# Optimization experiments

Hardware: AMD Instinct MI355X
Metric: run time of the kernel (lower is better)

## Reference

```python
import jax, jax.numpy as jnp
import numpy as np

N_EMBD = 768
N_HEAD = 12
EPS = 1e-5

def setup_inputs() -> dict:
    key = jax.random.key(0)
    ks = jax.random.split(key, 13)
    C = N_EMBD
    s = lambda n: 1.0 / np.sqrt(n)
    return {
        "x":      jax.random.normal(ks[0], (2, 2048, C), dtype=jnp.float32),
        "ln1_w":  jnp.ones((C,), jnp.float32),
        "ln1_b":  jnp.zeros((C,), jnp.float32),
        "w_qkv":  jax.random.normal(ks[1], (C, 3 * C), dtype=jnp.float32) * s(C),
        "b_qkv":  jnp.zeros((3 * C,), jnp.float32),
        "w_proj": jax.random.normal(ks[2], (C, C), dtype=jnp.float32) * s(C),
        "b_proj": jnp.zeros((C,), jnp.float32),
        "ln2_w":  jnp.ones((C,), jnp.float32),
        "ln2_b":  jnp.zeros((C,), jnp.float32),
        "w_fc1":  jax.random.normal(ks[3], (C, 4 * C), dtype=jnp.float32) * s(C),
        "b_fc1":  jnp.zeros((4 * C,), jnp.float32),
        "w_fc2":  jax.random.normal(ks[4], (4 * C, C), dtype=jnp.float32) * s(4 * C),
        "b_fc2":  jnp.zeros((C,), jnp.float32),
    }

def _layernorm(x, w, b):
    mu = jnp.mean(x, axis=-1, keepdims=True)
    var = jnp.mean(jnp.square(x - mu), axis=-1, keepdims=True)
    return (x - mu) * jax.lax.rsqrt(var + EPS) * w + b

def reference(x, ln1_w, ln1_b, w_qkv, b_qkv, w_proj, b_proj,
              ln2_w, ln2_b, w_fc1, b_fc1, w_fc2, b_fc2):
    B, T, C = x.shape
    H = N_HEAD
    hd = C // H
    # --- attention branch ---
    h = _layernorm(x, ln1_w, ln1_b)
    qkv = h @ w_qkv + b_qkv                                  # [B,T,3C]
    q, k, v = jnp.split(qkv, 3, axis=-1)
    q = q.reshape(B, T, H, hd).transpose(0, 2, 1, 3)          # [B,H,T,hd]
    k = k.reshape(B, T, H, hd).transpose(0, 2, 1, 3)
    v = v.reshape(B, T, H, hd).transpose(0, 2, 1, 3)
    att = jnp.einsum('bhqd,bhkd->bhqk', q, k) * (1.0 / np.sqrt(hd))
    causal = jnp.tril(jnp.ones((T, T), dtype=bool))
    att = jnp.where(causal, att, -jnp.inf)
    att = jax.nn.softmax(att, axis=-1)
    y = jnp.einsum('bhqk,bhkd->bhqd', att, v)                 # [B,H,T,hd]
    y = y.transpose(0, 2, 1, 3).reshape(B, T, C)
    x = x + (y @ w_proj + b_proj)
    # --- MLP branch (dropout = identity in eval) ---
    h = _layernorm(x, ln2_w, ln2_b)
    h = jax.nn.gelu(h @ w_fc1 + b_fc1, approximate=False)
    x = x + (h @ w_fc2 + b_fc2)
    return x
```

## Files before the change

kernel.cpp:

```cpp
#include <hip/hip_runtime.h>
#include <math.h>

typedef __attribute__((ext_vector_type(8))) short short8;
typedef __attribute__((ext_vector_type(4))) float floatx4;

__device__ __forceinline__ unsigned short f2bf(float f) {
    union { float f; unsigned u; } v; v.f = f;
    unsigned r = v.u + 0x7fffu + ((v.u >> 16) & 1u);
    return (unsigned short)(r >> 16);
}

__device__ __forceinline__ float bf2f(unsigned short h) {
    union { unsigned u; float f; } v; v.u = ((unsigned)h) << 16; return v.f;
}

__device__ __forceinline__ float fexp2(float x) {
#if __has_builtin(__builtin_amdgcn_exp2f)
    return __builtin_amdgcn_exp2f(x);
#else
    return __expf(x * 0.69314718056f);
#endif
}

__device__ __forceinline__ void gload16(const unsigned short* g, unsigned short* l) {
    __builtin_amdgcn_global_load_lds(
        (const __attribute__((address_space(1))) unsigned int*)g,
        (__attribute__((address_space(3))) unsigned int*)l, 16, 0, 0);
}

__global__ __launch_bounds__(256) void ln_kernel(const float* __restrict__ x,
                                                 const float* __restrict__ w,
                                                 const float* __restrict__ b,
                                                 unsigned short* __restrict__ o) {
    int row = blockIdx.x, tid = threadIdx.x;
    const float* xr = x + (size_t)row * 768;
    float v0 = xr[tid], v1 = xr[tid + 256], v2 = xr[tid + 512];
    float s = v0 + v1 + v2, ss = v0 * v0 + v1 * v1 + v2 * v2;
#pragma unroll
    for (int o_ = 32; o_; o_ >>= 1) { s += __shfl_xor(s, o_); ss += __shfl_xor(ss, o_); }
    __shared__ float red[8];
    if ((tid & 63) == 0) { red[tid >> 6] = s; red[(tid >> 6) + 4] = ss; }
    __syncthreads();
    s = red[0] + red[1] + red[2] + red[3];
    ss = red[4] + red[5] + red[6] + red[7];
    float mu = s * (1.f / 768.f);
    float var = ss * (1.f / 768.f) - mu * mu;
    float inv = rsqrtf(var + 1e-5f);
    unsigned short* orow = o + (size_t)row * 768;
    orow[tid]       = f2bf((v0 - mu) * inv * w[tid]       + b[tid]);
    orow[tid + 256] = f2bf((v1 - mu) * inv * w[tid + 256] + b[tid + 256]);
    orow[tid + 512] = f2bf((v2 - mu) * inv * w[tid + 512] + b[tid + 512]);
}

__global__ __launch_bounds__(256) void wt_all_kernel(
    const float* __restrict__ w0, unsigned short* __restrict__ t0,
    const float* __restrict__ w1, unsigned short* __restrict__ t1,
    const float* __restrict__ w2, unsigned short* __restrict__ t2,
    const float* __restrict__ w3, unsigned short* __restrict__ t3) {
    int bid = (int)blockIdx.x;
    const float* w; unsigned short* wt; int K, N, bx, by;
    if (bid < 1728)      { w = w0; wt = t0; K = 768;  N = 2304; int l = bid;        bx = l % 72; by = l / 72; }
    else if (bid < 2304) { w = w1; wt = t1; K = 768;  N = 768;  int l = bid - 1728; bx = l % 24; by = l / 24; }
    else if (bid < 4608) { w = w2; wt = t2; K = 768;  N = 3072; int l = bid - 2304; bx = l % 96; by = l / 96; }
    else                 { w = w3; wt = t3; K = 3072; N = 768;  int l = bid - 4608; bx = l % 24; by = l / 24; }
    __shared__ float t[32][33];
    int n0 = bx * 32, k0 = by * 32;
    int tx = threadIdx.x & 31, ty = threadIdx.x >> 5;
#pragma unroll
    for (int i = 0; i < 32; i += 8)
        t[ty + i][tx] = w[(size_t)(k0 + ty + i) * N + n0 + tx];
    __syncthreads();
#pragma unroll
    for (int i = 0; i < 32; i += 8)
        wt[(size_t)(n0 + ty + i) * K + k0 + tx] = f2bf(t[tx][ty + i]);
}

template <int EPI>
__global__ __launch_bounds__(256) void gemm_kernel(
    const unsigned short* __restrict__ A, const unsigned short* __restrict__ Bt,
    const float* __restrict__ bias, const float* __restrict__ resid,
    float* __restrict__ fout, unsigned short* __restrict__ o0,
    unsigned short* __restrict__ o1, unsigned short* __restrict__ o2,
    int K, int Kcnt) {
    __shared__ unsigned short Al[2][128 * 32];
    __shared__ unsigned short Bl[2][128 * 32];
    int tid = threadIdx.x, lane = tid & 63, w = tid >> 6;
    int wm = w >> 1, wn = w & 1;
    int nwg = (int)(gridDim.x * gridDim.y);
    int wgid = (int)(blockIdx.y * gridDim.x + blockIdx.x);
    int logical = (wgid & 7) * (nwg >> 3) + (wgid >> 3);
    int by = logical & 31, bx = logical >> 5;
    int m0 = by * 128;
    int n0, kof = 0, chunk = 0;
    if (EPI == 4) {
        n0 = (bx % 6) * 128;
        chunk = bx / 6;
        kof = chunk * 768;
    } else {
        n0 = bx * 128;
    }
    int lr = lane & 15, lk = (lane >> 4) << 3;

    int srow = w * 32 + (lane >> 2);
    int sko = (lane & 3) << 3;
    const unsigned short* Ab = A + (size_t)(m0 + srow) * K + kof + sko;
    const unsigned short* Bb = Bt + (size_t)(n0 + srow) * K + kof + sko;

    floatx4 acc[4][4];
#pragma unroll
    for (int i = 0; i < 4; i++)
#pragma unroll
        for (int j = 0; j < 4; j++) acc[i][j] = (floatx4){0.f, 0.f, 0.f, 0.f};

    int nk = Kcnt >> 5;
    auto stage = [&](int buf, int t) {
        int k0 = t << 5;
        unsigned short* Alp = &Al[buf][(w * 32) * 32];
        unsigned short* Blp = &Bl[buf][(w * 32) * 32];
        gload16(Ab + k0, Alp);
        gload16(Ab + 16 * K + k0, Alp + 16 * 32);
        gload16(Bb + k0, Blp);
        gload16(Bb + 16 * K + k0, Blp + 16 * 32);
    };

    stage(0, 0);
    for (int t = 0; t < nk; t++) {
        int cur = t & 1;
        __syncthreads();
        if (t + 1 < nk) stage(cur ^ 1, t + 1);
        short8 af[4], bfr[4];
#pragma unroll
        for (int mt = 0; mt < 4; mt++) af[mt] = *(short8*)&Al[cur][(wm * 64 + mt * 16 + lr) * 32 + lk];
#pragma unroll
        for (int nt = 0; nt < 4; nt++) bfr[nt] = *(short8*)&Bl[cur][(wn * 64 + nt * 16 + lr) * 32 + lk];
#pragma unroll
        for (int mt = 0; mt < 4; mt++)
#pragma unroll
            for (int nt = 0; nt < 4; nt++)
                acc[mt][nt] = __builtin_amdgcn_mfma_f32_16x16x32_bf16(af[mt], bfr[nt], acc[mt][nt], 0, 0, 0);
    }

    int mb = m0 + wm * 64, nb = n0 + wn * 64;
    int sec = 0;
    if (EPI == 0) sec = n0 / 768;
#pragma unroll
    for (int mt = 0; mt < 4; mt++)
#pragma unroll
        for (int nt = 0; nt < 4; nt++)
#pragma unroll
            for (int r = 0; r < 4; r++) {
                int mrow = mb + mt * 16 + ((lane >> 4) << 2) + r;
                int ncol = nb + nt * 16 + lr;
                float val = acc[mt][nt][r];
                if (EPI != 4) val += bias[ncol];
                if (EPI == 0) {
                    int f = ncol - sec * 768;
                    int h = f >> 6, d = f & 63;
                    int bb = mrow >> 11, t = mrow & 2047;
                    if (sec == 0)
                        o0[((size_t)(bb * 12 + h) * 2048 + t) * 64 + d] = f2bf(val * 0.1803368801f);
                    else if (sec == 1)
                        o1[((size_t)(bb * 12 + h) * 2048 + t) * 64 + d] = f2bf(val);
                    else
                        o2[((size_t)(bb * 12 + h) * 64 + d) * 2048 + t] = f2bf(val);
                } else if (EPI == 1) {
                    fout[(size_t)mrow * 768 + ncol] = val + resid[(size_t)mrow * 768 + ncol];
                } else if (EPI == 2) {
                    float g = 0.5f * val * (1.f + erff(val * 0.70710678118f));
                    o0[(size_t)mrow * 3072 + ncol] = f2bf(g);
                } else {
                    unsigned short* op = (chunk == 0) ? o0 : (chunk == 1) ? o1
                                       : (chunk == 2) ? o2 : (unsigned short*)fout;
                    op[(size_t)mrow * 768 + ncol] = f2bf(val);
                }
            }
}

__global__ __launch_bounds__(256) void fc2_combine(
    const unsigned short* __restrict__ p0, const unsigned short* __restrict__ p1,
    const unsigned short* __restrict__ p2, const unsigned short* __restrict__ p3,
    const float* __restrict__ bias, const float* __restrict__ resid,
    float* __restrict__ out) {
    int i = blockIdx.x * 256 + threadIdx.x;
    size_t base = (size_t)i * 8;
    int col = (int)(base % 768);
    short8 a0 = *(const short8*)&p0[base];
    short8 a1 = *(const short8*)&p1[base];
    short8 a2 = *(const short8*)&p2[base];
    short8 a3 = *(const short8*)&p3[base];
#pragma unroll
    for (int j = 0; j < 8; j++) {
        float s = bf2f((unsigned short)a0[j]) + bf2f((unsigned short)a1[j]) +
                  bf2f((unsigned short)a2[j]) + bf2f((unsigned short)a3[j]);
        out[base + j] = s + bias[col + j] + resid[base + j];
    }
}

__global__ __launch_bounds__(256) void attn_kernel(const unsigned short* __restrict__ q_s,
                                                   const unsigned short* __restrict__ k_s,
                                                   const unsigned short* __restrict__ v_t,
                                                   unsigned short* __restrict__ y,
                                                   unsigned short* __restrict__ opart,
                                                   float* __restrict__ lpart) {
    __shared__ unsigned short KVs[2][4096];
    __shared__ unsigned short Pls[4][32][72];
    const int T = 2048, H = 12;
    int tid = threadIdx.x, lane = tid & 63, w = tid >> 6;
    int xx = (int)blockIdx.x;
    int bq, c;
    if (xx < 16)      { c = 0; bq = xx; }
    else if (xx < 28) { c = 1; bq = xx - 12; }
    else if (xx < 36) { c = 2; bq = xx - 20; }
    else              { c = 3; bq = xx - 24; }
    int bh = blockIdx.y;
    int bi = bh / H, hh = bh - bi * H;
    const unsigned short* qp = q_s + (size_t)bh * T * 64;
    const unsigned short* kp = k_s + (size_t)bh * T * 64;
    const unsigned short* vp = v_t + (size_t)bh * 64 * T;
    int wq0 = bq * 128 + w * 32;
    int lr = lane & 15, lk8 = (lane >> 4) << 3, hi = lane >> 4;
    int nt_blk = 2 * bq + 2;
    int t0 = c * 8;
    int t1 = t0 + 8 < nt_blk ? t0 + 8 : nt_blk;

    unsigned short (*Pl)[72] = Pls[w];

    int srow = tid >> 3, ssl = tid & 7;

    auto stage = [&](int buf, int t) {
        int kv0 = t * 64;
        unsigned short* base = &KVs[buf][(tid >> 6) * 512];
#pragma unroll
        for (int h = 0; h < 2; h++) {
            int r = srow + h * 32;
            int ss = ssl ^ (r & 7);
            gload16(kp + (size_t)(kv0 + r) * 64 + ss * 8, base + h * 2048);
        }
    };

    short8 aq[2][2];
#pragma unroll
    for (int mt = 0; mt < 2; mt++)
#pragma unroll
        for (int kf = 0; kf < 2; kf++)
            aq[mt][kf] = *(const short8*)&qp[(size_t)(wq0 + mt * 16 + lr) * 64 + kf * 32 + lk8];

    floatx4 yacc[2][4];
    float lacc[2][4];
#pragma unroll
    for (int i = 0; i < 2; i++)
#pragma unroll
        for (int j = 0; j < 4; j++) {
            yacc[i][j] = (floatx4){0.f, 0.f, 0.f, 0.f};
            lacc[i][j] = 0.f;
        }

    stage(0, t0);
    __syncthreads();

    for (int t = t0; t < t1; t++) {
        int cur = (t - t0) & 1;
        if (t + 1 < t1) stage(cur ^ 1, t + 1);
        int kv0 = t * 64;
        if (kv0 <= wq0 + 31) {
            const unsigned short* Kt = &KVs[cur][0];
            floatx4 sacc[2][4];
#pragma unroll
            for (int i = 0; i < 2; i++)
#pragma unroll
                for (int j = 0; j < 4; j++) sacc[i][j] = (floatx4){0.f, 0.f, 0.f, 0.f};
#pragma unroll
            for (int kf = 0; kf < 2; kf++) {
                int sl = ((kf << 2) | hi) ^ (lr & 7);
                short8 bk[4];
#pragma unroll
                for (int nt = 0; nt < 4; nt++)
                    bk[nt] = *(const short8*)&Kt[(nt * 16 + lr) * 64 + sl * 8];
#pragma unroll
                for (int mt = 0; mt < 2; mt++)
#pragma unroll
                    for (int nt = 0; nt < 4; nt++)
                        sacc[mt][nt] = __builtin_amdgcn_mfma_f32_16x16x32_bf16(aq[mt][kf], bk[nt], sacc[mt][nt], 0, 0, 0);
            }
            short8 bv[4][2];
#pragma unroll
            for (int nt = 0; nt < 4; nt++)
#pragma unroll
                for (int kf = 0; kf < 2; kf++)
                    bv[nt][kf] = *(const short8*)&vp[(size_t)(nt * 16 + lr) * T + kv0 + kf * 32 + lk8];
            bool full = (kv0 + 63 <= wq0);
#pragma unroll
            for (int mt = 0; mt < 2; mt++)
#pragma unroll
                for (int r = 0; r < 4; r++) {
                    int qg = wq0 + mt * 16 + (hi << 2) + r;
                    int prow = mt * 16 + (hi << 2) + r;
#pragma unroll
                    for (int nt = 0; nt < 4; nt++) {
                        float sv = sacc[mt][nt][r];
                        if (!full) {
                            int kvg = kv0 + nt * 16 + lr;
                            sv = (kvg <= qg) ? sv : -1e30f;
                        }
                        float p = fexp2(sv);
                        lacc[mt][r] += p;
                        Pl[prow][nt * 16 + lr] = f2bf(p);
                    }
                }
#pragma unroll
            for (int kf = 0; kf < 2; kf++) {
                short8 pa[2];
#pragma unroll
                for (int mt = 0; mt < 2; mt++) pa[mt] = *(short8*)&Pl[mt * 16 + lr][kf * 32 + lk8];
#pragma unroll
                for (int mt = 0; mt < 2; mt++)
#pragma unroll
                    for (int nt = 0; nt < 4; nt++)
                        yacc[mt][nt] = __builtin_amdgcn_mfma_f32_16x16x32_bf16(pa[mt], bv[nt][kf], yacc[mt][nt], 0, 0, 0);
            }
        }
        __syncthreads();
    }

    if (bq < 4) {
#pragma unroll
        for (int mt = 0; mt < 2; mt++)
#pragma unroll
            for (int r = 0; r < 4; r++) {
                float l = lacc[mt][r];
                l += __shfl_xor(l, 1);
                l += __shfl_xor(l, 2);
                l += __shfl_xor(l, 4);
                l += __shfl_xor(l, 8);
                float inv = 1.f / l;
                int qg = wq0 + mt * 16 + (hi << 2) + r;
#pragma unroll
                for (int nt = 0; nt < 4; nt++)
                    y[((size_t)(bi * T + qg)) * 768 + hh * 64 + nt * 16 + lr] = f2bf(yacc[mt][nt][r] * inv);
            }
    } else {
        int g = bq >> 2, rr = bq & 3;
        int base = (g == 1) ? 2 * rr : (g == 2) ? 8 + 3 * rr : 20 + 4 * rr;
        int slab = bh * 36 + base + c;
        unsigned short* op = opart + (size_t)slab * 8192;
        float* lp = lpart + (size_t)slab * 128;
#pragma unroll
        for (int mt = 0; mt < 2; mt++)
#pragma unroll
            for (int r = 0; r < 4; r++) {
                float l = lacc[mt][r];
                l += __shfl_xor(l, 1);
                l += __shfl_xor(l, 2);
                l += __shfl_xor(l, 4);
                l += __shfl_xor(l, 8);
                int wrow = w * 32 + mt * 16 + (hi << 2) + r;
                if (lr == 0) lp[wrow] = l;
#pragma unroll
                for (int nt = 0; nt < 4; nt++)
                    op[(size_t)wrow * 64 + nt * 16 + lr] = f2bf(yacc[mt][nt][r]);
            }
    }
}

__global__ __launch_bounds__(256) void attn_combine(const unsigned short* __restrict__ opart,
                                                    const float* __restrict__ lpart,
                                                    unsigned short* __restrict__ y) {
    const int T = 2048, H = 12;
    int bq = 4 + (int)blockIdx.x;
    int bh = blockIdx.y;
    int bi = bh / H, hh = bh - bi * H;
    int nchunk = (bq >> 2) + 1;
    int g = bq >> 2, rr = bq & 3;
    int base = (g == 1) ? 2 * rr : (g == 2) ? 8 + 3 * rr : 20 + 4 * rr;
    int tid = threadIdx.x;
    int row = tid >> 1, cb = (tid & 1) * 32;

    float l = 0.f;
    for (int c = 0; c < nchunk; c++) l += lpart[(size_t)(bh * 36 + base + c) * 128 + row];
    float inv = 1.f / l;

    float s[32];
#pragma unroll
    for (int j = 0; j < 32; j++) s[j] = 0.f;
    for (int c = 0; c < nchunk; c++) {
        const unsigned short* op = opart + ((size_t)(bh * 36 + base + c) * 128 + row) * 64 + cb;
#pragma unroll
        for (int v = 0; v < 4; v++) {
            short8 ob = *(const short8*)&op[v * 8];
#pragma unroll
            for (int j = 0; j < 8; j++) s[v * 8 + j] += bf2f((unsigned short)ob[j]);
        }
    }
    int qg = bq * 128 + row;
    unsigned short* yr = y + ((size_t)(bi * T + qg)) * 768 + hh * 64 + cb;
#pragma unroll
    for (int v = 0; v < 4; v++) {
        short8 ob;
#pragma unroll
        for (int j = 0; j < 8; j++) ob[j] = (short)f2bf(s[v * 8 + j] * inv);
        *(short8*)&yr[v * 8] = ob;
    }
}

extern "C" void kernel_launch(void* const* d_in, const int* in_sizes, int n_in,
                              void* d_out, int out_size, void* d_ws, size_t ws_size,
                              hipStream_t stream) {
    const float* x    = (const float*)d_in[0];
    const float* ln1w = (const float*)d_in[1];
    const float* ln1b = (const float*)d_in[2];
    const float* wqkv = (const float*)d_in[3];
    const float* bqkv = (const float*)d_in[4];
    const float* wproj= (const float*)d_in[5];
    const float* bproj= (const float*)d_in[6];
    const float* ln2w = (const float*)d_in[7];
    const float* ln2b = (const float*)d_in[8];
    const float* wfc1 = (const float*)d_in[9];
    const float* bfc1 = (const float*)d_in[10];
    const float* wfc2 = (const float*)d_in[11];
    const float* bfc2 = (const float*)d_in[12];
    float* out = (float*)d_out;

    char* ws = (char*)d_ws;
    size_t off = 0;
    auto alloc = [&](size_t bytes) { void* p = ws + off; off += (bytes + 255) & ~(size_t)255; return p; };

    const size_t MT = 4096;
    unsigned short* wqkv_t = (unsigned short*)alloc(2304 * 768 * 2);
    unsigned short* wproj_t= (unsigned short*)alloc(768 * 768 * 2);
    unsigned short* wfc1_t = (unsigned short*)alloc(3072 * 768 * 2);
    unsigned short* wfc2_t = (unsigned short*)alloc(768 * 3072 * 2);
    unsigned short* h12    = (unsigned short*)alloc(MT * 768 * 2);
    float*          x1     = (float*)alloc(MT * 768 * 4);
    unsigned short* qs     = (unsigned short*)alloc(MT * 768 * 2);
    unsigned short* ks     = (unsigned short*)alloc(MT * 768 * 2);
    unsigned short* vt     = (unsigned short*)alloc(MT * 768 * 2);
    unsigned short* yb     = (unsigned short*)alloc(MT * 768 * 2);
    unsigned short* hm     = qs;
    unsigned short* opart  = (unsigned short*)alloc(24 * 36 * 8192 * 2);
    float*          lpart  = (float*)alloc(24 * 36 * 128 * 4);

    unsigned short* p0 = (unsigned short*)ws;
    unsigned short* p1 = opart;
    unsigned short* p2 = (unsigned short*)((char*)opart + (size_t)MT * 768 * 2);
    unsigned short* p3 = h12;

    wt_all_kernel<<<dim3(6912), 256, 0, stream>>>(wqkv, wqkv_t, wproj, wproj_t,
                                                  wfc1, wfc1_t, wfc2, wfc2_t);

    ln_kernel<<<4096, 256, 0, stream>>>(x, ln1w, ln1b, h12);
    gemm_kernel<0><<<dim3(18, 32), 256, 0, stream>>>(h12, wqkv_t, bqkv, nullptr, nullptr, qs, ks, vt, 768, 768);
    attn_kernel<<<dim3(40, 24), 256, 0, stream>>>(qs, ks, vt, yb, opart, lpart);
    attn_combine<<<dim3(12, 24), 256, 0, stream>>>(opart, lpart, yb);
    gemm_kernel<1><<<dim3(6, 32), 256, 0, stream>>>(yb, wproj_t, bproj, x, x1, nullptr, nullptr, nullptr, 768, 768);
    ln_kernel<<<4096, 256, 0, stream>>>(x1, ln2w, ln2b, h12);
    gemm_kernel<2><<<dim3(24, 32), 256, 0, stream>>>(h12, wfc1_t, bfc1, nullptr, nullptr, hm, nullptr, nullptr, 768, 768);
    gemm_kernel<4><<<dim3(24, 32), 256, 0, stream>>>(hm, wfc2_t, nullptr, nullptr, (float*)p3, p0, p1, p2, 3072, 768);
    fc2_combine<<<dim3(1536), 256, 0, stream>>>(p0, p1, p2, p3, bfc2, x1, out);
}
```

Baseline: 211.9 us.

## Add 256x256 eight-wave pipelined GEMM for QKV, FC1 and FC2

```diff
diff --git a/kernel.cpp b/kernel.cpp
--- a/kernel.cpp
+++ b/kernel.cpp
@@ -27,6 +27,10 @@
         (const __attribute__((address_space(1))) unsigned int*)g,
         (__attribute__((address_space(3))) unsigned int*)l, 16, 0, 0);
 }
+
+#define MBAR  __builtin_amdgcn_s_barrier()
+#define LGKM0 do { asm volatile("s_waitcnt lgkmcnt(0)" ::: "memory"); __builtin_amdgcn_sched_barrier(0); } while (0)
+#define VMC(n) asm volatile("s_waitcnt vmcnt(" #n ")" ::: "memory")
 
 __global__ __launch_bounds__(256) void ln_kernel(const float* __restrict__ x,
                                                  const float* __restrict__ w,
@@ -79,9 +83,7 @@
 __global__ __launch_bounds__(256) void gemm_kernel(
     const unsigned short* __restrict__ A, const unsigned short* __restrict__ Bt,
     const float* __restrict__ bias, const float* __restrict__ resid,
-    float* __restrict__ fout, unsigned short* __restrict__ o0,
-    unsigned short* __restrict__ o1, unsigned short* __restrict__ o2,
-    int K, int Kcnt) {
+    float* __restrict__ fout, int K, int Kcnt) {
     __shared__ unsigned short Al[2][128 * 32];
     __shared__ unsigned short Bl[2][128 * 32];
     int tid = threadIdx.x, lane = tid & 63, w = tid >> 6;
@@ -90,21 +92,13 @@
     int wgid = (int)(blockIdx.y * gridDim.x + blockIdx.x);
     int logical = (wgid & 7) * (nwg >> 3) + (wgid >> 3);
     int by = logical & 31, bx = logical >> 5;
-    int m0 = by * 128;
-    int n0, kof = 0, chunk = 0;
-    if (EPI == 4) {
-        n0 = (bx % 6) * 128;
-        chunk = bx / 6;
-        kof = chunk * 768;
-    } else {
-        n0 = bx * 128;
-    }
+    int m0 = by * 128, n0 = bx * 128;
     int lr = lane & 15, lk = (lane >> 4) << 3;
 
     int srow = w * 32 + (lane >> 2);
     int sko = (lane & 3) << 3;
-    const unsigned short* Ab = A + (size_t)(m0 + srow) * K + kof + sko;
-    const unsigned short* Bb = Bt + (size_t)(n0 + srow) * K + kof + sko;
+    const unsigned short* Ab = A + (size_t)(m0 + srow) * K + sko;
+    const unsigned short* Bb = Bt + (size_t)(n0 + srow) * K + sko;
 
     floatx4 acc[4][4];
 #pragma unroll
@@ -141,8 +135,6 @@
     }
 
     int mb = m0 + wm * 64, nb = n0 + wn * 64;
-    int sec = 0;
-    if (EPI == 0) sec = n0 / 768;
 #pragma unroll
     for (int mt = 0; mt < 4; mt++)
 #pragma unroll
@@ -151,7 +143,139 @@
             for (int r = 0; r < 4; r++) {
                 int mrow = mb + mt * 16 + ((lane >> 4) << 2) + r;
                 int ncol = nb + nt * 16 + lr;
-                float val = acc[mt][nt][r];
+                float val = acc[mt][nt][r] + bias[ncol];
+                fout[(size_t)mrow * 768 + ncol] = val + resid[(size_t)mrow * 768 + ncol];
+            }
+}
+
+template <int EPI>
+__global__ __launch_bounds__(512, 2) void gemm8p_kernel(
+    const unsigned short* __restrict__ A, const unsigned short* __restrict__ Bt,
+    const float* __restrict__ bias, float* __restrict__ fout,
+    unsigned short* __restrict__ o0, unsigned short* __restrict__ o1,
+    unsigned short* __restrict__ o2, int K, int Kcnt) {
+    extern __shared__ unsigned short lds[];
+    int tid = threadIdx.x, lane = tid & 63, w = tid >> 6;
+    int wm = w >> 2, wn = w & 3;
+    int lr = lane & 15, hi = lane >> 4;
+    int nwg = (int)(gridDim.x * gridDim.y);
+    int wgid = (int)(blockIdx.y * gridDim.x + blockIdx.x);
+    int q = nwg >> 3, r = nwg & 7;
+    int xcd = wgid & 7, idx = wgid >> 3;
+    int logical = (xcd < r ? xcd * (q + 1) : r * (q + 1) + (xcd - r) * q) + idx;
+    int my = (int)gridDim.y;
+    int by = logical % my, bx = logical / my;
+    int m0 = by * 256;
+    int n0, kof = 0, chunk = 0;
+    if (EPI == 4) { n0 = (bx % 3) * 256; chunk = bx / 3; kof = chunk * 768; }
+    else n0 = bx * 256;
+
+    int sw = (lane & 7) ^ ((lane >> 3) & 7);
+    int pk0 = hi ^ (lr & 7), pk1 = (hi + 4) ^ (lr & 7);
+
+    auto stageA = [&](int dbuf, int kt, int mh) {
+#pragma unroll
+        for (int j = 0; j < 2; j++) {
+            int rowbase = mh * 64 + j * 128 + w * 8;
+            gload16(A + (size_t)(m0 + rowbase + (lane >> 3)) * K + kof + kt * 64 + sw * 8,
+                    lds + dbuf * 32768 + rowbase * 64);
+        }
+    };
+    auto stageB = [&](int dbuf, int kt, int nh) {
+#pragma unroll
+        for (int j = 0; j < 2; j++) {
+            int rowbase = nh * 32 + (2 * j + (w >> 2)) * 64 + (w & 3) * 8;
+            gload16(Bt + (size_t)(n0 + rowbase + (lane >> 3)) * K + kof + kt * 64 + sw * 8,
+                    lds + dbuf * 32768 + 16384 + rowbase * 64);
+        }
+    };
+
+    floatx4 acc[8][4];
+#pragma unroll
+    for (int i = 0; i < 8; i++)
+#pragma unroll
+        for (int j = 0; j < 4; j++) acc[i][j] = (floatx4){0.f, 0.f, 0.f, 0.f};
+    short8 af[4][2], bfA[2][2], bfB[2][2];
+
+    auto loadA = [&](int dbuf, int mh) {
+        const unsigned short* base = lds + dbuf * 32768 + (wm * 128 + mh * 64 + lr) * 64;
+#pragma unroll
+        for (int mt = 0; mt < 4; mt++) {
+            af[mt][0] = *(const short8*)(base + mt * 1024 + pk0 * 8);
+            af[mt][1] = *(const short8*)(base + mt * 1024 + pk1 * 8);
+        }
+    };
+    auto loadB = [&](int dbuf, int nh, short8 (&bf)[2][2]) {
+        const unsigned short* base = lds + dbuf * 32768 + 16384 + (wn * 64 + nh * 32 + lr) * 64;
+#pragma unroll
+        for (int nt = 0; nt < 2; nt++) {
+            bf[nt][0] = *(const short8*)(base + nt * 1024 + pk0 * 8);
+            bf[nt][1] = *(const short8*)(base + nt * 1024 + pk1 * 8);
+        }
+    };
+    auto mma = [&](short8 (&bf)[2][2], int mh, int nh) {
+        __builtin_amdgcn_s_setprio(1);
+#pragma unroll
+        for (int mt = 0; mt < 4; mt++)
+#pragma unroll
+            for (int nt = 0; nt < 2; nt++)
+#pragma unroll
+                for (int kk = 0; kk < 2; kk++)
+                    acc[mh * 4 + mt][nh * 2 + nt] = __builtin_amdgcn_mfma_f32_16x16x32_bf16(
+                        af[mt][kk], bf[nt][kk], acc[mh * 4 + mt][nh * 2 + nt], 0, 0, 0);
+        __builtin_amdgcn_s_setprio(0);
+    };
+
+    int nkt = Kcnt >> 6;
+    int niter = nkt >> 1;
+
+    stageA(0, 0, 0); stageA(0, 0, 1); stageB(0, 0, 0); stageB(0, 0, 1);
+    if (1 < nkt) { stageA(1, 1, 0); stageB(1, 1, 1); VMC(4); }
+    else VMC(0);
+    MBAR;
+
+    for (int i = 0; i < niter; i++) {
+        int t1 = 2 * i + 1, t2 = 2 * i + 2, t3 = 2 * i + 3;
+        bool s2 = t2 < nkt, s3 = t3 < nkt;
+        loadA(0, 0); loadB(0, 0, bfA);
+        stageA(1, t1, 1);
+        MBAR; LGKM0; mma(bfA, 0, 0); MBAR;
+        loadB(0, 1, bfB);
+        stageB(1, t1, 0);
+        MBAR; LGKM0; mma(bfB, 0, 1); MBAR;
+        loadA(0, 1);
+        if (s2) stageA(0, t2, 0);
+        MBAR; LGKM0; mma(bfB, 1, 1); MBAR;
+        if (s2) stageB(0, t2, 1);
+        MBAR; LGKM0; mma(bfA, 1, 0);
+        if (s2) VMC(4); else VMC(0);
+        MBAR;
+        loadA(1, 0); loadB(1, 0, bfA);
+        if (s2) stageA(0, t2, 1);
+        MBAR; LGKM0; mma(bfA, 0, 0); MBAR;
+        loadB(1, 1, bfB);
+        if (s2) stageB(0, t2, 0);
+        MBAR; LGKM0; mma(bfB, 0, 1); MBAR;
+        loadA(1, 1);
+        if (s3) stageA(1, t3, 0);
+        MBAR; LGKM0; mma(bfB, 1, 1); MBAR;
+        if (s3) stageB(1, t3, 1);
+        MBAR; LGKM0; mma(bfA, 1, 0);
+        if (i + 1 < niter) VMC(4); else VMC(0);
+        MBAR;
+    }
+
+    int mbase = m0 + wm * 128, nbase = n0 + wn * 64;
+    int sec = (EPI == 0) ? n0 / 768 : 0;
+#pragma unroll
+    for (int mt = 0; mt < 8; mt++)
+#pragma unroll
+        for (int nt = 0; nt < 4; nt++)
+#pragma unroll
+            for (int rr = 0; rr < 4; rr++) {
+                int mrow = mbase + mt * 16 + hi * 4 + rr;
+                int ncol = nbase + nt * 16 + lr;
+                float val = acc[mt][nt][rr];
                 if (EPI != 4) val += bias[ncol];
                 if (EPI == 0) {
                     int f = ncol - sec * 768;
@@ -163,8 +287,6 @@
                         o1[((size_t)(bb * 12 + h) * 2048 + t) * 64 + d] = f2bf(val);
                     else
                         o2[((size_t)(bb * 12 + h) * 64 + d) * 2048 + t] = f2bf(val);
-                } else if (EPI == 1) {
-                    fout[(size_t)mrow * 768 + ncol] = val + resid[(size_t)mrow * 768 + ncol];
                 } else if (EPI == 2) {
                     float g = 0.5f * val * (1.f + erff(val * 0.70710678118f));
                     o0[(size_t)mrow * 3072 + ncol] = f2bf(g);
@@ -224,7 +346,6 @@
     int t1 = t0 + 8 < nt_blk ? t0 + 8 : nt_blk;
 
     unsigned short (*Pl)[72] = Pls[w];
-
     int srow = tid >> 3, ssl = tid & 7;
 
     auto stage = [&](int buf, int t) {
@@ -444,16 +565,23 @@
     unsigned short* p2 = (unsigned short*)((char*)opart + (size_t)MT * 768 * 2);
     unsigned short* p3 = h12;
 
+    hipFuncSetAttribute(reinterpret_cast<const void*>(gemm8p_kernel<0>),
+                        hipFuncAttributeMaxDynamicSharedMemorySize, 131072);
+    hipFuncSetAttribute(reinterpret_cast<const void*>(gemm8p_kernel<2>),
+                        hipFuncAttributeMaxDynamicSharedMemorySize, 131072);
+    hipFuncSetAttribute(reinterpret_cast<const void*>(gemm8p_kernel<4>),
+                        hipFuncAttributeMaxDynamicSharedMemorySize, 131072);
+
     wt_all_kernel<<<dim3(6912), 256, 0, stream>>>(wqkv, wqkv_t, wproj, wproj_t,
                                                   wfc1, wfc1_t, wfc2, wfc2_t);
 
     ln_kernel<<<4096, 256, 0, stream>>>(x, ln1w, ln1b, h12);
-    gemm_kernel<0><<<dim3(18, 32), 256, 0, stream>>>(h12, wqkv_t, bqkv, nullptr, nullptr, qs, ks, vt, 768, 768);
+    gemm8p_kernel<0><<<dim3(9, 16), 512, 131072, stream>>>(h12, wqkv_t, bqkv, nullptr, qs, ks, vt, 768, 768);
     attn_kernel<<<dim3(40, 24), 256, 0, stream>>>(qs, ks, vt, yb, opart, lpart);
     attn_combine<<<dim3(12, 24), 256, 0, stream>>>(opart, lpart, yb);
-    gemm_kernel<1><<<dim3(6, 32), 256, 0, stream>>>(yb, wproj_t, bproj, x, x1, nullptr, nullptr, nullptr, 768, 768);
+    gemm_kernel<1><<<dim3(6, 32), 256, 0, stream>>>(yb, wproj_t, bproj, x, x1, 768, 768);
     ln_kernel<<<4096, 256, 0, stream>>>(x1, ln2w, ln2b, h12);
-    gemm_kernel<2><<<dim3(24, 32), 256, 0, stream>>>(h12, wfc1_t, bfc1, nullptr, nullptr, hm, nullptr, nullptr, 768, 768);
-    gemm_kernel<4><<<dim3(24, 32), 256, 0, stream>>>(hm, wfc2_t, nullptr, nullptr, (float*)p3, p0, p1, p2, 3072, 768);
+    gemm8p_kernel<2><<<dim3(12, 16), 512, 131072, stream>>>(h12, wfc1_t, bfc1, nullptr, hm, nullptr, nullptr, 768, 768);
+    gemm8p_kernel<4><<<dim3(12, 16), 512, 131072, stream>>>(hm, wfc2_t, nullptr, (float*)p3, p0, p1, p2, 3072, 768);
     fc2_combine<<<dim3(1536), 256, 0, stream>>>(p0, p1, p2, p3, bfc2, x1, out);
 }
```

Result: slower. 224.6 us (+6.0%).

## Halve attention split-K chunk size and split-K the output projection GEMM

Applied to the files above, without the earlier changes.

```diff
diff --git a/kernel.cpp b/kernel.cpp
--- a/kernel.cpp
+++ b/kernel.cpp
@@ -95,7 +95,7 @@
     if (EPI == 4) {
         n0 = (bx % 6) * 128;
         chunk = bx / 6;
-        kof = chunk * 768;
+        kof = chunk * Kcnt;
     } else {
         n0 = bx * 128;
     }
@@ -163,12 +163,10 @@
                         o1[((size_t)(bb * 12 + h) * 2048 + t) * 64 + d] = f2bf(val);
                     else
                         o2[((size_t)(bb * 12 + h) * 64 + d) * 2048 + t] = f2bf(val);
-                } else if (EPI == 1) {
-                    fout[(size_t)mrow * 768 + ncol] = val + resid[(size_t)mrow * 768 + ncol];
                 } else if (EPI == 2) {
                     float g = 0.5f * val * (1.f + erff(val * 0.70710678118f));
                     o0[(size_t)mrow * 3072 + ncol] = f2bf(g);
-                } else {
+                } else if (EPI == 4) {
                     unsigned short* op = (chunk == 0) ? o0 : (chunk == 1) ? o1
                                        : (chunk == 2) ? o2 : (unsigned short*)fout;
                     op[(size_t)mrow * 768 + ncol] = f2bf(val);
@@ -176,7 +174,7 @@
             }
 }
 
-__global__ __launch_bounds__(256) void fc2_combine(
+__global__ __launch_bounds__(256) void sk_combine(
     const unsigned short* __restrict__ p0, const unsigned short* __restrict__ p1,
     const unsigned short* __restrict__ p2, const unsigned short* __restrict__ p3,
     const float* __restrict__ bias, const float* __restrict__ resid,
@@ -196,6 +194,7 @@
     }
 }
 
+template <int CH>
 __global__ __launch_bounds__(256) void attn_kernel(const unsigned short* __restrict__ q_s,
                                                    const unsigned short* __restrict__ k_s,
                                                    const unsigned short* __restrict__ v_t,
@@ -205,13 +204,17 @@
     __shared__ unsigned short KVs[2][4096];
     __shared__ unsigned short Pls[4][32][72];
     const int T = 2048, H = 12;
+    const int SLABS = (CH == 8) ? 36 : 70;
+    const int NDIR  = (CH == 8) ? 4 : 2;
     int tid = threadIdx.x, lane = tid & 63, w = tid >> 6;
     int xx = (int)blockIdx.x;
-    int bq, c;
-    if (xx < 16)      { c = 0; bq = xx; }
-    else if (xx < 28) { c = 1; bq = xx - 12; }
-    else if (xx < 36) { c = 2; bq = xx - 20; }
-    else              { c = 3; bq = xx - 24; }
+    int bq = 0, acc = 0;
+    while (true) {
+        int n = (2 * bq + 2 + CH - 1) / CH;
+        if (acc + n > xx) break;
+        acc += n; bq++;
+    }
+    int c = xx - acc;
     int bh = blockIdx.y;
     int bi = bh / H, hh = bh - bi * H;
     const unsigned short* qp = q_s + (size_t)bh * T * 64;
@@ -220,11 +223,10 @@
     int wq0 = bq * 128 + w * 32;
     int lr = lane & 15, lk8 = (lane >> 4) << 3, hi = lane >> 4;
     int nt_blk = 2 * bq + 2;
-    int t0 = c * 8;
-    int t1 = t0 + 8 < nt_blk ? t0 + 8 : nt_blk;
+    int t0 = c * CH;
+    int t1 = t0 + CH < nt_blk ? t0 + CH : nt_blk;
 
     unsigned short (*Pl)[72] = Pls[w];
-
     int srow = tid >> 3, ssl = tid & 7;
 
     auto stage = [&](int buf, int t) {
@@ -322,7 +324,7 @@
         __syncthreads();
     }
 
-    if (bq < 4) {
+    if (nt_blk <= CH) {
 #pragma unroll
         for (int mt = 0; mt < 2; mt++)
 #pragma unroll
@@ -339,9 +341,7 @@
                     y[((size_t)(bi * T + qg)) * 768 + hh * 64 + nt * 16 + lr] = f2bf(yacc[mt][nt][r] * inv);
             }
     } else {
-        int g = bq >> 2, rr = bq & 3;
-        int base = (g == 1) ? 2 * rr : (g == 2) ? 8 + 3 * rr : 20 + 4 * rr;
-        int slab = bh * 36 + base + c;
+        int slab = bh * SLABS + (acc - NDIR) + c;
         unsigned short* op = opart + (size_t)slab * 8192;
         float* lp = lpart + (size_t)slab * 128;
 #pragma unroll
@@ -362,28 +362,31 @@
     }
 }
 
+template <int CH>
 __global__ __launch_bounds__(256) void attn_combine(const unsigned short* __restrict__ opart,
                                                     const float* __restrict__ lpart,
                                                     unsigned short* __restrict__ y) {
     const int T = 2048, H = 12;
-    int bq = 4 + (int)blockIdx.x;
+    const int SLABS = (CH == 8) ? 36 : 70;
+    const int BQ0   = (CH == 8) ? 4 : 2;
+    int bq = BQ0 + (int)blockIdx.x;
     int bh = blockIdx.y;
     int bi = bh / H, hh = bh - bi * H;
-    int nchunk = (bq >> 2) + 1;
-    int g = bq >> 2, rr = bq & 3;
-    int base = (g == 1) ? 2 * rr : (g == 2) ? 8 + 3 * rr : 20 + 4 * rr;
+    int nchunk = (2 * bq + 2 + CH - 1) / CH;
+    int base = 0;
+    for (int b = BQ0; b < bq; b++) base += (2 * b + 2 + CH - 1) / CH;
     int tid = threadIdx.x;
     int row = tid >> 1, cb = (tid & 1) * 32;
 
     float l = 0.f;
-    for (int c = 0; c < nchunk; c++) l += lpart[(size_t)(bh * 36 + base + c) * 128 + row];
+    for (int c = 0; c < nchunk; c++) l += lpart[(size_t)(bh * SLABS + base + c) * 128 + row];
     float inv = 1.f / l;
 
     float s[32];
 #pragma unroll
     for (int j = 0; j < 32; j++) s[j] = 0.f;
     for (int c = 0; c < nchunk; c++) {
-        const unsigned short* op = opart + ((size_t)(bh * 36 + base + c) * 128 + row) * 64 + cb;
+        const unsigned short* op = opart + ((size_t)(bh * SLABS + base + c) * 128 + row) * 64 + cb;
 #pragma unroll
         for (int v = 0; v < 4; v++) {
             short8 ob = *(const short8*)&op[v * 8];
@@ -436,24 +439,35 @@
     unsigned short* vt     = (unsigned short*)alloc(MT * 768 * 2);
     unsigned short* yb     = (unsigned short*)alloc(MT * 768 * 2);
     unsigned short* hm     = qs;
-    unsigned short* opart  = (unsigned short*)alloc(24 * 36 * 8192 * 2);
-    float*          lpart  = (float*)alloc(24 * 36 * 128 * 4);
+    float*          lpart  = (float*)alloc((size_t)24 * 70 * 128 * 4);
+    unsigned short* opart  = (unsigned short*)alloc((size_t)24 * 70 * 8192 * 2);
+    bool ch4 = (off <= ws_size);
 
     unsigned short* p0 = (unsigned short*)ws;
     unsigned short* p1 = opart;
     unsigned short* p2 = (unsigned short*)((char*)opart + (size_t)MT * 768 * 2);
     unsigned short* p3 = h12;
+    unsigned short* q0 = qs;
+    unsigned short* q1 = ks;
+    unsigned short* q2 = vt;
+    unsigned short* q3 = h12;
 
     wt_all_kernel<<<dim3(6912), 256, 0, stream>>>(wqkv, wqkv_t, wproj, wproj_t,
                                                   wfc1, wfc1_t, wfc2, wfc2_t);
 
     ln_kernel<<<4096, 256, 0, stream>>>(x, ln1w, ln1b, h12);
     gemm_kernel<0><<<dim3(18, 32), 256, 0, stream>>>(h12, wqkv_t, bqkv, nullptr, nullptr, qs, ks, vt, 768, 768);
-    attn_kernel<<<dim3(40, 24), 256, 0, stream>>>(qs, ks, vt, yb, opart, lpart);
-    attn_combine<<<dim3(12, 24), 256, 0, stream>>>(opart, lpart, yb);
-    gemm_kernel<1><<<dim3(6, 32), 256, 0, stream>>>(yb, wproj_t, bproj, x, x1, nullptr, nullptr, nullptr, 768, 768);
+    if (ch4) {
+        attn_kernel<4><<<dim3(72, 24), 256, 0, stream>>>(qs, ks, vt, yb, opart, lpart);
+        attn_combine<4><<<dim3(14, 24), 256, 0, stream>>>(opart, lpart, yb);
+    } else {
+        attn_kernel<8><<<dim3(40, 24), 256, 0, stream>>>(qs, ks, vt, yb, opart, lpart);
+        attn_combine<8><<<dim3(12, 24), 256, 0, stream>>>(opart, lpart, yb);
+    }
+    gemm_kernel<4><<<dim3(24, 32), 256, 0, stream>>>(yb, wproj_t, nullptr, nullptr, (float*)q3, q0, q1, q2, 768, 192);
+    sk_combine<<<dim3(1536), 256, 0, stream>>>(q0, q1, q2, q3, bproj, x, x1);
     ln_kernel<<<4096, 256, 0, stream>>>(x1, ln2w, ln2b, h12);
     gemm_kernel<2><<<dim3(24, 32), 256, 0, stream>>>(h12, wfc1_t, bfc1, nullptr, nullptr, hm, nullptr, nullptr, 768, 768);
     gemm_kernel<4><<<dim3(24, 32), 256, 0, stream>>>(hm, wfc2_t, nullptr, nullptr, (float*)p3, p0, p1, p2, 3072, 768);
-    fc2_combine<<<dim3(1536), 256, 0, stream>>>(p0, p1, p2, p3, bfc2, x1, out);
-}
+    sk_combine<<<dim3(1536), 256, 0, stream>>>(p0, p1, p2, p3, bfc2, x1, out);
+}
```

Result: slower. 220.7 us (+4.1%).
